# Kernel optimization log

Measured on AMD Instinct MI355X. Metric: run time of the kernel, lower is better.

The kernel has to match this reference:

```python
import jax, jax.numpy as jnp
import numpy as np


def _conv2d(x, w, b):
    # NCHW valid conv, kernel shape OIHW
    y = jax.lax.conv_general_dilated(x, w, (1, 1), 'VALID',
                                     dimension_numbers=('NCHW', 'OIHW', 'NCHW'))
    return y + b[None, :, None, None]


def _rgcn(x, src, dst, edge_type, root, rel, bias):
    # PyG RGCNConv: out_i = x_i @ root + bias + sum_r mean_{j in N_r(i)} x_j @ W_r
    # x: [B, N, F]; src/dst: [E]; rel: [R, F, F]
    out = x @ root + bias
    N = x.shape[1]
    for r in range(rel.shape[0]):  # small fixed relation count
        m = (edge_type == r).astype(x.dtype)                # [E]
        msg = (x @ rel[r])[:, src] * m[None, :, None]       # [B, E, F]
        agg = jnp.zeros_like(out).at[:, dst].add(msg)       # [B, N, F]
        cnt = jnp.zeros((N,), x.dtype).at[dst].add(m)       # per-node relation degree
        out = out + agg / jnp.clip(cnt, 1.0)[None, :, None]
    return out


def setup_inputs() -> dict:
    key = jax.random.key(0)
    ks = jax.random.split(key, 16)
    B, C, N, T = 16, 3, 3000, 50
    E, R, S, F = 96000, 3, 500, 43  # F = 2*20 + 3
    observation = jax.random.normal(ks[0], (B, C, N, T), jnp.float32)
    last_action = jax.random.uniform(ks[1], (B, S + 1), dtype=jnp.float32)
    edge_index = jax.random.randint(ks[2], (2, E), 0, N, jnp.int32)
    edge_type = jax.random.randint(ks[3], (E,), 0, R, jnp.int32)
    nodes_to_select = jnp.sort(jax.random.randint(ks[4], (S,), 0, N, jnp.int32))

    def w(k, shape, fan_in):
        return jax.random.normal(k, shape, jnp.float32) / np.sqrt(fan_in).astype(np.float32)

    params = dict(
        ws1=w(ks[5], (3, 3, 1, 3), 9), bs1=jnp.zeros(3, jnp.float32),
        ws2=w(ks[6], (20, 3, 1, 48), 144), bs2=jnp.zeros(20, jnp.float32),
        wm1=w(ks[7], (3, 3, 1, 21), 63), bm1=jnp.zeros(3, jnp.float32),
        wm2=w(ks[8], (20, 3, 1, 30), 90), bm2=jnp.zeros(20, jnp.float32),
        root1=w(ks[9], (F, F), F), rel1=w(ks[10], (R, F, F), F), bias1=jnp.zeros(F, jnp.float32),
        root2=w(ks[11], (F, F), F), rel2=w(ks[12], (R, F, F), F), bias2=jnp.zeros(F, jnp.float32),
        wf=w(ks[13], (1, 87, 1, 1), 87), bf=jnp.zeros(1, jnp.float32),
    )
    return {"observation": observation, "last_action": last_action,
            "edge_index": edge_index, "edge_type": edge_type,
            "nodes_to_select": nodes_to_select, **params}


def reference(observation, last_action, edge_index, edge_type, nodes_to_select,
              ws1, bs1, ws2, bs2, wm1, bm1, wm2, bm2,
              root1, rel1, bias1, root2, rel2, bias2, wf, bf):
    relu = jax.nn.relu
    B = observation.shape[0]
    last_stocks = last_action[:, 1:][:, None, :, None]                      # [B,1,S,1]
    short = relu(_conv2d(relu(_conv2d(observation, ws1, bs1)), ws2, bs2))   # [B,20,N,1]
    mid = relu(_conv2d(relu(_conv2d(observation, wm1, bm1)), wm2, bm2))     # [B,20,N,1]
    longf = relu(jnp.max(observation, axis=3, keepdims=True))               # [B,3,N,1]
    temporal = jnp.concatenate([short, mid, longf], axis=1)                 # [B,43,N,1]
    x = jnp.transpose(temporal[..., 0], (0, 2, 1))                          # [B,N,43]
    src, dst = edge_index[0], edge_index[1]
    h = jax.nn.leaky_relu(_rgcn(x, src, dst, edge_type, root1, rel1, bias1), 0.01)
    h = jax.nn.leaky_relu(_rgcn(h, src, dst, edge_type, root2, rel2, bias2), 0.01)
    graph_features = jnp.transpose(h, (0, 2, 1))[..., None]                 # [B,43,N,1]
    feats = jnp.concatenate([temporal, graph_features], axis=1)             # [B,86,N,1]
    feats = feats[:, :, nodes_to_select, :]                                 # [B,86,S,1]
    feats = jnp.concatenate([last_stocks, feats], axis=1)                   # [B,87,S,1]
    out = _conv2d(feats, wf, bf)                                            # [B,1,S,1]
    cash = jnp.zeros((B, 1, 1, 1), out.dtype)  # cash bias zeroed in mu()
    logits = jnp.concatenate([cash, out], axis=2)[:, 0, :, 0]               # [B,S+1]
    return jax.nn.softmax(logits, axis=-1)  # softmax_temperature = 1
```

## Files before the change

kernel.cpp:

```cpp
#include <hip/hip_runtime.h>
#include <math.h>

#define NB 16
#define NC 3
#define NN 3000
#define NT 50
#define NE 96000
#define NR 3
#define NS 500
#define NF 43
#define NFP 44
#define NBF (NB*NFP)
#define NBKT (NR*NN)
#define CAP 96

#define XT_OFF   0
#define H1_OFF   (XT_OFF + NN*NBF)
#define LG_OFF   (H1_OFF + NN*NBF)
#define INT_BASE (LG_OFF + NB*(NS+1))
#define CNT_OFF  0
#define EBUF_OFF (CNT_OFF + NBKT)

__global__ __launch_bounds__(256, 3) void k_front(
    const float* __restrict__ obs,
    const float* __restrict__ ws1, const float* __restrict__ bs1,
    const float* __restrict__ ws2, const float* __restrict__ bs2,
    const float* __restrict__ wm1, const float* __restrict__ bm1,
    const float* __restrict__ wm2, const float* __restrict__ bm2,
    float* __restrict__ x,
    const int* __restrict__ ei, const int* __restrict__ et,
    int* __restrict__ cnt, int* __restrict__ ebuf)
{
    __shared__ float sp[4][64][23];
    int tid = threadIdx.x;

    if (blockIdx.x >= 1500) {
        int e = (blockIdx.x - 1500) * 256 + tid;
        int bkt = et[e] * NN + ei[NE + e];
        int pos = atomicAdd(&cnt[bkt], 1);
        if (pos < CAP) ebuf[bkt * CAP + pos] = ei[e];
        return;
    }

    int wave = __builtin_amdgcn_readfirstlane(tid >> 6);
    int lane = tid & 63;

    if (blockIdx.x < 750) {
        int idx = blockIdx.x * 64 + lane;
        int b = idx / NN, n = idx - b * NN;
        float wS[3][14];
        int base = 12 * wave;
        #pragma unroll
        for (int c = 0; c < 3; ++c) {
            const float2* p2 = (const float2*)(obs + ((size_t)(b * NC + c) * NN + n) * NT + base);
            #pragma unroll
            for (int jj = 0; jj < 7; ++jj) {
                float2 u = p2[jj];
                wS[c][2 * jj] = u.x; wS[c][2 * jj + 1] = u.y;
            }
        }
        float acc[20];
        #pragma unroll
        for (int o = 0; o < 20; ++o) acc[o] = 0.f;
        #pragma unroll
        for (int j = 0; j < 12; ++j) {
            float y[3];
            #pragma unroll
            for (int c = 0; c < 3; ++c) {
                float s = bs1[c];
                #pragma unroll
                for (int i = 0; i < 3; ++i)
                    #pragma unroll
                    for (int k = 0; k < 3; ++k)
                        s = fmaf(wS[i][j + k], ws1[(c * 3 + i) * 3 + k], s);
                y[c] = fmaxf(s, 0.f);
            }
            int gt = base + j;
            #pragma unroll
            for (int o = 0; o < 20; ++o) {
                float a = acc[o];
                #pragma unroll
                for (int c = 0; c < 3; ++c)
                    a = fmaf(y[c], ws2[(o * 3 + c) * 48 + gt], a);
                acc[o] = a;
            }
        }
        #pragma unroll
        for (int o = 0; o < 20; ++o) sp[wave][lane][o] = acc[o];
        __syncthreads();
        #pragma unroll
        for (int q = 0; q < 5; ++q) {
            int item = q * 256 + tid;
            int node = item / 20, o = item - node * 20;
            int g = blockIdx.x * 64 + node;
            int bb = g / NN, nn = g - bb * NN;
            float s = ((sp[0][node][o] + sp[1][node][o]) +
                       (sp[2][node][o] + sp[3][node][o])) + bs2[o];
            x[(size_t)nn * NBF + bb * NFP + o] = fmaxf(s, 0.f);
        }
        return;
    }

    {
        int idx = (blockIdx.x - 750) * 64 + lane;
        int b = idx / NN, n = idx - b * NN;
        int mbase = (wave < 3) ? 8 * wave : 24;
        int nld   = (wave < 3) ? 14 : 13;
        const float* orow = obs + ((size_t)b * NC * NN + n) * NT + mbase;

        float s[3][8];
        #pragma unroll
        for (int c = 0; c < 3; ++c)
            #pragma unroll
            for (int t = 0; t < 8; ++t) s[c][t] = bm1[c];
        float cmax[3];
        float wA[28], wB[28];

        #define LOADW(buf, ch)                                                  \
        {                                                                       \
            const float2* p2 = (const float2*)(orow + (size_t)(ch) * NN * NT);  \
            _Pragma("unroll")                                                   \
            for (int jj = 0; jj < 14; ++jj) {                                   \
                if (jj < nld) {                                                 \
                    float2 u = p2[jj];                                          \
                    buf[2 * jj] = u.x; buf[2 * jj + 1] = u.y;                   \
                } else { buf[2 * jj] = 0.f; buf[2 * jj + 1] = 0.f; }            \
            }                                                                   \
        }
        #define COMPW(buf, ii)                                                  \
        {                                                                       \
            float m = buf[0];                                                   \
            _Pragma("unroll")                                                   \
            for (int t = 1; t < 28; ++t) m = fmaxf(m, buf[t]);                  \
            cmax[ii] = m;                                                       \
            _Pragma("unroll")                                                   \
            for (int c = 0; c < 3; ++c)                                         \
                _Pragma("unroll")                                               \
                for (int t = 0; t < 8; ++t) {                                   \
                    float a = s[c][t];                                          \
                    _Pragma("unroll")                                           \
                    for (int k = 0; k < 21; ++k)                                \
                        a = fmaf(buf[t + k], wm1[(c * 3 + (ii)) * 21 + k], a);  \
                    s[c][t] = a;                                                \
                }                                                               \
        }

        LOADW(wA, 0)
        LOADW(wB, 1)
        COMPW(wA, 0)
        LOADW(wA, 2)
        COMPW(wB, 1)
        COMPW(wA, 2)
        #undef LOADW
        #undef COMPW

        float acc[20];
        #pragma unroll
        for (int o = 0; o < 20; ++o) acc[o] = 0.f;
        int cntM = (wave < 3) ? 8 : 6;
        #pragma unroll
        for (int j = 0; j < 8; ++j) {
            if (j < cntM) {
                float y0 = fmaxf(s[0][j], 0.f);
                float y1 = fmaxf(s[1][j], 0.f);
                float y2 = fmaxf(s[2][j], 0.f);
                int gt = mbase + j;
                #pragma unroll
                for (int o = 0; o < 20; ++o) {
                    float a = acc[o];
                    a = fmaf(y0, wm2[(o * 3 + 0) * 30 + gt], a);
                    a = fmaf(y1, wm2[(o * 3 + 1) * 30 + gt], a);
                    a = fmaf(y2, wm2[(o * 3 + 2) * 30 + gt], a);
                    acc[o] = a;
                }
            }
        }
        #pragma unroll
        for (int o = 0; o < 20; ++o) sp[wave][lane][o] = acc[o];
        #pragma unroll
        for (int c = 0; c < 3; ++c) sp[wave][lane][20 + c] = cmax[c];
    }
    __syncthreads();
    #pragma unroll
    for (int q = 0; q < 6; ++q) {
        int item = q * 256 + tid;
        if (item < 1472) {
            int node = item / 23, o = item - node * 23;
            int g = (blockIdx.x - 750) * 64 + node;
            int bb = g / NN, nn = g - bb * NN;
            size_t row = (size_t)nn * NBF + bb * NFP;
            if (o < 20) {
                float s = ((sp[0][node][o] + sp[1][node][o]) +
                           (sp[2][node][o] + sp[3][node][o])) + bm2[o];
                x[row + 20 + o] = fmaxf(s, 0.f);
            } else {
                float m = fmaxf(fmaxf(sp[0][node][o], sp[1][node][o]),
                                fmaxf(sp[2][node][o], sp[3][node][o]));
                x[row + 40 + (o - 20)] = fmaxf(m, 0.f);
            }
        }
    }
}

template<bool LEAKY, bool SEL>
__global__ __launch_bounds__(256) void k_rgcn(
    const float* __restrict__ in, const float* __restrict__ xsrc,
    const int* __restrict__ cnt, const int* __restrict__ ebuf,
    const int* __restrict__ sel,
    const float* __restrict__ root, const float* __restrict__ rel,
    const float* __restrict__ bias,
    const float* __restrict__ la, const float* __restrict__ wf,
    const float* __restrict__ bf,
    float* __restrict__ out)
{
    __shared__ float lrow[4][NBF];
    __shared__ float sP[8][4][NFP];

    int tid = threadIdx.x;
    int wave = __builtin_amdgcn_readfirstlane(tid >> 6);
    int lane = tid & 63;
    int i = blockIdx.x;
    int node = __builtin_amdgcn_readfirstlane(SEL ? sel[i] : i);

    const float* wbase = (wave == 0) ? root : (rel + (size_t)(wave - 1) * NF * NF);
    float wsl[43];
    #pragma unroll
    for (int j = 0; j < 43; ++j)
        wsl[j] = (lane < NF) ? wbase[j * NF + lane] : 0.f;

    if (wave == 3) {
        #pragma unroll
        for (int j = 0; j < 11; ++j) {
            float v = in[(size_t)node * NBF + j * 64 + lane];
            if (LEAKY) v = v >= 0.f ? v : 0.01f * v;
            lrow[0][j * 64 + lane] = v;
        }
    } else {
        int bkt = wave * NN + node;
        int cvr = __builtin_amdgcn_readfirstlane(cnt[bkt]);
        float ic = 1.0f / fmaxf((float)cvr, 1.0f);
        int cv = cvr > CAP ? CAP : cvr;
        const int* eb = ebuf + bkt * CAP;

        float acc[11];
        #pragma unroll
        for (int j = 0; j < 11; ++j) acc[j] = 0.f;

        for (int e = 0; e < cv; e += 4) {
            int4 q = *(const int4*)(eb + e);
            int m = cv - e;
            {
                const float* p = in + (size_t)__builtin_amdgcn_readfirstlane(q.x) * NBF;
                #pragma unroll
                for (int j = 0; j < 11; ++j) {
                    float v = p[j * 64 + lane];
                    if (LEAKY) v = v >= 0.f ? v : 0.01f * v;
                    acc[j] += v;
                }
            }
            if (m > 1) {
                const float* p = in + (size_t)__builtin_amdgcn_readfirstlane(q.y) * NBF;
                #pragma unroll
                for (int j = 0; j < 11; ++j) {
                    float v = p[j * 64 + lane];
                    if (LEAKY) v = v >= 0.f ? v : 0.01f * v;
                    acc[j] += v;
                }
            }
            if (m > 2) {
                const float* p = in + (size_t)__builtin_amdgcn_readfirstlane(q.z) * NBF;
                #pragma unroll
                for (int j = 0; j < 11; ++j) {
                    float v = p[j * 64 + lane];
                    if (LEAKY) v = v >= 0.f ? v : 0.01f * v;
                    acc[j] += v;
                }
            }
            if (m > 3) {
                const float* p = in + (size_t)__builtin_amdgcn_readfirstlane(q.w) * NBF;
                #pragma unroll
                for (int j = 0; j < 11; ++j) {
                    float v = p[j * 64 + lane];
                    if (LEAKY) v = v >= 0.f ? v : 0.01f * v;
                    acc[j] += v;
                }
            }
        }
        #pragma unroll
        for (int j = 0; j < 11; ++j) lrow[wave + 1][j * 64 + lane] = acc[j] * ic;
    }
    __syncthreads();

    for (int h = 0; h < 2; ++h) {
        #pragma unroll
        for (int rr = 0; rr < 8; ++rr) {
            int b = h * 8 + rr;
            const float4* a4 = (const float4*)&lrow[wave][b * NFP];
            float a0 = 0.f, a1 = 0.f, a2 = 0.f, a3 = 0.f;
            #pragma unroll
            for (int c = 0; c < 10; ++c) {
                float4 v = a4[c];
                a0 = fmaf(v.x, wsl[4 * c], a0);
                a1 = fmaf(v.y, wsl[4 * c + 1], a1);
                a2 = fmaf(v.z, wsl[4 * c + 2], a2);
                a3 = fmaf(v.w, wsl[4 * c + 3], a3);
            }
            {
                float4 v = a4[10];
                a0 = fmaf(v.x, wsl[40], a0);
                a1 = fmaf(v.y, wsl[41], a1);
                a2 = fmaf(v.z, wsl[42], a2);
            }
            if (lane < NF) sP[rr][wave][lane] = (a0 + a1) + (a2 + a3);
        }
        __syncthreads();

        int r0 = 2 * wave, r1 = 2 * wave + 1;
        int b0 = h * 8 + r0, b1 = h * 8 + r1;
        if (!SEL) {
            if (lane < NF) {
                float bi_ = bias[lane];
                float s0 = ((sP[r0][0][lane] + sP[r0][1][lane]) +
                            (sP[r0][2][lane] + sP[r0][3][lane])) + bi_;
                float s1 = ((sP[r1][0][lane] + sP[r1][1][lane]) +
                            (sP[r1][2][lane] + sP[r1][3][lane])) + bi_;
                out[(size_t)i * NBF + b0 * NFP + lane] = s0;
                out[(size_t)i * NBF + b1 * NFP + lane] = s1;
            }
        } else {
            float p0 = 0.f, p1 = 0.f;
            if (lane < NF) {
                float bi_ = bias[lane];
                float s0 = ((sP[r0][0][lane] + sP[r0][1][lane]) +
                            (sP[r0][2][lane] + sP[r0][3][lane])) + bi_;
                float s1 = ((sP[r1][0][lane] + sP[r1][1][lane]) +
                            (sP[r1][2][lane] + sP[r1][3][lane])) + bi_;
                s0 = s0 >= 0.f ? s0 : 0.01f * s0;
                s1 = s1 >= 0.f ? s1 : 0.01f * s1;
                float x0 = xsrc[(size_t)node * NBF + b0 * NFP + lane];
                float x1 = xsrc[(size_t)node * NBF + b1 * NFP + lane];
                p0 = fmaf(wf[44 + lane], s0, wf[1 + lane] * x0);
                p1 = fmaf(wf[44 + lane], s1, wf[1 + lane] * x1);
            }
            #pragma unroll
            for (int o = 32; o > 0; o >>= 1) {
                p0 += __shfl_down(p0, o);
                p1 += __shfl_down(p1, o);
            }
            if (lane == 0) {
                out[(size_t)b0 * (NS + 1) + 1 + i] =
                    p0 + bf[0] + wf[0] * la[b0 * (NS + 1) + 1 + i];
                out[(size_t)b1 * (NS + 1) + 1 + i] =
                    p1 + bf[0] + wf[0] * la[b1 * (NS + 1) + 1 + i];
            }
        }
        __syncthreads();
    }
}

__device__ inline float wred_max(float v) {
    #pragma unroll
    for (int o = 32; o > 0; o >>= 1) v = fmaxf(v, __shfl_down(v, o));
    return v;
}
__device__ inline float wred_sum(float v) {
    #pragma unroll
    for (int o = 32; o > 0; o >>= 1) v += __shfl_down(v, o);
    return v;
}

__global__ __launch_bounds__(512) void k_softmax(
    const float* __restrict__ lg, float* __restrict__ out)
{
    __shared__ float sred[8];
    __shared__ float sbc[2];
    int b = blockIdx.x, tid = threadIdx.x;

    float val = -3.0e38f;
    if (tid <= NS) val = (tid == 0) ? 0.f : lg[(size_t)b * (NS + 1) + tid];

    float m = wred_max(val);
    if ((tid & 63) == 0) sred[tid >> 6] = m;
    __syncthreads();
    if (tid == 0) {
        float mm = sred[0];
        #pragma unroll
        for (int i = 1; i < 8; ++i) mm = fmaxf(mm, sred[i]);
        sbc[0] = mm;
    }
    __syncthreads();
    float mx = sbc[0];
    float e = (tid <= NS) ? expf(val - mx) : 0.f;
    float s = wred_sum(e);
    if ((tid & 63) == 0) sred[tid >> 6] = s;
    __syncthreads();
    if (tid == 0) {
        float t = 0.f;
        #pragma unroll
        for (int i = 0; i < 8; ++i) t += sred[i];
        sbc[1] = t;
    }
    __syncthreads();
    if (tid <= NS) out[(size_t)b * (NS + 1) + tid] = e / sbc[1];
}

extern "C" void kernel_launch(void* const* d_in, const int* in_sizes, int n_in,
                              void* d_out, int out_size, void* d_ws, size_t ws_size,
                              hipStream_t stream)
{
    const float* obs   = (const float*)d_in[0];
    const float* la    = (const float*)d_in[1];
    const int*   ei    = (const int*)d_in[2];
    const int*   et    = (const int*)d_in[3];
    const int*   nodes = (const int*)d_in[4];
    const float* ws1 = (const float*)d_in[5],  *bs1 = (const float*)d_in[6];
    const float* ws2 = (const float*)d_in[7],  *bs2 = (const float*)d_in[8];
    const float* wm1 = (const float*)d_in[9],  *bm1 = (const float*)d_in[10];
    const float* wm2 = (const float*)d_in[11], *bm2 = (const float*)d_in[12];
    const float* root1 = (const float*)d_in[13], *rel1 = (const float*)d_in[14], *bias1 = (const float*)d_in[15];
    const float* root2 = (const float*)d_in[16], *rel2 = (const float*)d_in[17], *bias2 = (const float*)d_in[18];
    const float* wf = (const float*)d_in[19], *bf = (const float*)d_in[20];

    float* wsp = (float*)d_ws;
    float* x   = wsp + XT_OFF;
    float* h1  = wsp + H1_OFF;
    float* lg  = wsp + LG_OFF;
    int*   ibase = (int*)(wsp + INT_BASE);
    int*   cnt   = ibase + CNT_OFF;
    int*   ebuf  = ibase + EBUF_OFF;

    hipMemsetAsync(cnt, 0, NBKT * sizeof(int), stream);

    k_front<<<1875, 256, 0, stream>>>(
        obs, ws1, bs1, ws2, bs2, wm1, bm1, wm2, bm2, x, ei, et, cnt, ebuf);

    k_rgcn<false, false><<<NN, 256, 0, stream>>>(
        x, nullptr, cnt, ebuf, nullptr, root1, rel1, bias1,
        nullptr, nullptr, nullptr, h1);

    k_rgcn<true, true><<<NS, 256, 0, stream>>>(
        h1, x, cnt, ebuf, nodes, root2, rel2, bias2,
        la, wf, bf, lg);

    k_softmax<<<NB, 512, 0, stream>>>(lg, (float*)d_out);
}
```

Before: 210.3 us.

## Split neighbor aggregation across all waves and fuse softmax into last RGCN block

Previously one wave per relation gathered whole neighbor rows while the fourth wave only loaded the self row. Now all four waves share every relation's gather, each lane covering up to three columns of the 704-wide row and looping over the relations, which balances load across waves. The separate softmax kernel is removed. The last block of the selected-node RGCN, detected by an atomic counter plus threadfence, computes the softmax directly. This saves a launch at the cost of a serialized tail block and an extra counter in the memset.

```diff
diff --git a/kernel.cpp b/kernel.cpp
--- a/kernel.cpp
+++ b/kernel.cpp
@@ -19,7 +19,8 @@
 #define LG_OFF   (H1_OFF + NN*NBF)
 #define INT_BASE (LG_OFF + NB*(NS+1))
 #define CNT_OFF  0
-#define EBUF_OFF (CNT_OFF + NBKT)
+#define DONE_OFF NBKT
+#define EBUF_OFF (NBKT + 4)
 
 __global__ __launch_bounds__(256, 3) void k_front(
     const float* __restrict__ obs,
@@ -211,10 +212,12 @@
     const float* __restrict__ bias,
     const float* __restrict__ la, const float* __restrict__ wf,
     const float* __restrict__ bf,
-    float* __restrict__ out)
+    float* __restrict__ out, int* __restrict__ done,
+    float* __restrict__ res)
 {
     __shared__ float lrow[4][NBF];
     __shared__ float sP[8][4][NFP];
+    __shared__ int slast;
 
     int tid = threadIdx.x;
     int wave = __builtin_amdgcn_readfirstlane(tid >> 6);
@@ -228,67 +231,60 @@
     for (int j = 0; j < 43; ++j)
         wsl[j] = (lane < NF) ? wbase[j * NF + lane] : 0.f;
 
-    if (wave == 3) {
-        #pragma unroll
-        for (int j = 0; j < 11; ++j) {
-            float v = in[(size_t)node * NBF + j * 64 + lane];
-            if (LEAKY) v = v >= 0.f ? v : 0.01f * v;
-            lrow[0][j * 64 + lane] = v;
-        }
-    } else {
-        int bkt = wave * NN + node;
+    int base = wave * 64 + lane;
+    bool has3 = (wave < 3);
+
+    #define ACT(v) (LEAKY ? ((v) >= 0.f ? (v) : 0.01f * (v)) : (v))
+    {
+        const float* p = in + (size_t)node * NBF;
+        float v0 = p[base], v1 = p[base + 256];
+        float v2 = has3 ? p[base + 512] : 0.f;
+        lrow[0][base] = ACT(v0);
+        lrow[0][base + 256] = ACT(v1);
+        if (has3) lrow[0][base + 512] = ACT(v2);
+    }
+    #pragma unroll 1
+    for (int r = 0; r < NR; ++r) {
+        int bkt = r * NN + node;
         int cvr = __builtin_amdgcn_readfirstlane(cnt[bkt]);
         float ic = 1.0f / fmaxf((float)cvr, 1.0f);
         int cv = cvr > CAP ? CAP : cvr;
         const int* eb = ebuf + bkt * CAP;
 
-        float acc[11];
-        #pragma unroll
-        for (int j = 0; j < 11; ++j) acc[j] = 0.f;
-
+        float a0 = 0.f, a1 = 0.f, a2 = 0.f;
         for (int e = 0; e < cv; e += 4) {
             int4 q = *(const int4*)(eb + e);
             int m = cv - e;
             {
                 const float* p = in + (size_t)__builtin_amdgcn_readfirstlane(q.x) * NBF;
-                #pragma unroll
-                for (int j = 0; j < 11; ++j) {
-                    float v = p[j * 64 + lane];
-                    if (LEAKY) v = v >= 0.f ? v : 0.01f * v;
-                    acc[j] += v;
-                }
+                float u0 = p[base], u1 = p[base + 256];
+                a0 += ACT(u0); a1 += ACT(u1);
+                if (has3) { float u2 = p[base + 512]; a2 += ACT(u2); }
             }
             if (m > 1) {
                 const float* p = in + (size_t)__builtin_amdgcn_readfirstlane(q.y) * NBF;
-                #pragma unroll
-                for (int j = 0; j < 11; ++j) {
-                    float v = p[j * 64 + lane];
-                    if (LEAKY) v = v >= 0.f ? v : 0.01f * v;
-                    acc[j] += v;
-                }
+                float u0 = p[base], u1 = p[base + 256];
+                a0 += ACT(u0); a1 += ACT(u1);
+                if (has3) { float u2 = p[base + 512]; a2 += ACT(u2); }
             }
             if (m > 2) {
                 const float* p = in + (size_t)__builtin_amdgcn_readfirstlane(q.z) * NBF;
-                #pragma unroll
-                for (int j = 0; j < 11; ++j) {
-                    float v = p[j * 64 + lane];
-                    if (LEAKY) v = v >= 0.f ? v : 0.01f * v;
-                    acc[j] += v;
-                }
+                float u0 = p[base], u1 = p[base + 256];
+                a0 += ACT(u0); a1 += ACT(u1);
+                if (has3) { float u2 = p[base + 512]; a2 += ACT(u2); }
             }
             if (m > 3) {
                 const float* p = in + (size_t)__builtin_amdgcn_readfirstlane(q.w) * NBF;
-                #pragma unroll
-                for (int j = 0; j < 11; ++j) {
-                    float v = p[j * 64 + lane];
-                    if (LEAKY) v = v >= 0.f ? v : 0.01f * v;
-                    acc[j] += v;
-                }
-            }
-        }
-        #pragma unroll
-        for (int j = 0; j < 11; ++j) lrow[wave + 1][j * 64 + lane] = acc[j] * ic;
-    }
+                float u0 = p[base], u1 = p[base + 256];
+                a0 += ACT(u0); a1 += ACT(u1);
+                if (has3) { float u2 = p[base + 512]; a2 += ACT(u2); }
+            }
+        }
+        lrow[r + 1][base] = a0 * ic;
+        lrow[r + 1][base + 256] = a1 * ic;
+        if (has3) lrow[r + 1][base + 512] = a2 * ic;
+    }
+    #undef ACT
     __syncthreads();
 
     for (int h = 0; h < 2; ++h) {
@@ -356,52 +352,46 @@
         }
         __syncthreads();
     }
-}
-
-__device__ inline float wred_max(float v) {
-    #pragma unroll
-    for (int o = 32; o > 0; o >>= 1) v = fmaxf(v, __shfl_down(v, o));
-    return v;
-}
-__device__ inline float wred_sum(float v) {
-    #pragma unroll
-    for (int o = 32; o > 0; o >>= 1) v += __shfl_down(v, o);
-    return v;
-}
-
-__global__ __launch_bounds__(512) void k_softmax(
-    const float* __restrict__ lg, float* __restrict__ out)
-{
-    __shared__ float sred[8];
-    __shared__ float sbc[2];
-    int b = blockIdx.x, tid = threadIdx.x;
-
-    float val = -3.0e38f;
-    if (tid <= NS) val = (tid == 0) ? 0.f : lg[(size_t)b * (NS + 1) + tid];
-
-    float m = wred_max(val);
-    if ((tid & 63) == 0) sred[tid >> 6] = m;
-    __syncthreads();
-    if (tid == 0) {
-        float mm = sred[0];
-        #pragma unroll
-        for (int i = 1; i < 8; ++i) mm = fmaxf(mm, sred[i]);
-        sbc[0] = mm;
-    }
-    __syncthreads();
-    float mx = sbc[0];
-    float e = (tid <= NS) ? expf(val - mx) : 0.f;
-    float s = wred_sum(e);
-    if ((tid & 63) == 0) sred[tid >> 6] = s;
-    __syncthreads();
-    if (tid == 0) {
-        float t = 0.f;
-        #pragma unroll
-        for (int i = 0; i < 8; ++i) t += sred[i];
-        sbc[1] = t;
-    }
-    __syncthreads();
-    if (tid <= NS) out[(size_t)b * (NS + 1) + tid] = e / sbc[1];
+
+    if (SEL) {
+        __threadfence();
+        if (tid == 0) {
+            int old = atomicAdd(done, 1);
+            slast = (old == NS - 1) ? 1 : 0;
+        }
+        __syncthreads();
+        if (slast) {
+            __threadfence();
+            for (int bb = wave; bb < NB; bb += 4) {
+                const float* l = out + (size_t)bb * (NS + 1);
+                float vals[8]; float mx = -3.0e38f;
+                #pragma unroll
+                for (int k = 0; k < 8; ++k) {
+                    int idx = k * 64 + lane;
+                    float v = (idx == 0) ? 0.f
+                            : ((idx <= NS) ? l[idx] : -3.0e38f);
+                    vals[k] = v; mx = fmaxf(mx, v);
+                }
+                #pragma unroll
+                for (int o = 32; o > 0; o >>= 1) mx = fmaxf(mx, __shfl_xor(mx, o));
+                float ev[8]; float se = 0.f;
+                #pragma unroll
+                for (int k = 0; k < 8; ++k) {
+                    int idx = k * 64 + lane;
+                    float e = (idx <= NS) ? expf(vals[k] - mx) : 0.f;
+                    ev[k] = e; se += e;
+                }
+                #pragma unroll
+                for (int o = 32; o > 0; o >>= 1) se += __shfl_xor(se, o);
+                float inv = 1.f / se;
+                #pragma unroll
+                for (int k = 0; k < 8; ++k) {
+                    int idx = k * 64 + lane;
+                    if (idx <= NS) res[(size_t)bb * (NS + 1) + idx] = ev[k] * inv;
+                }
+            }
+        }
+    }
 }
 
 extern "C" void kernel_launch(void* const* d_in, const int* in_sizes, int n_in,
@@ -427,20 +417,19 @@
     float* lg  = wsp + LG_OFF;
     int*   ibase = (int*)(wsp + INT_BASE);
     int*   cnt   = ibase + CNT_OFF;
+    int*   done  = ibase + DONE_OFF;
     int*   ebuf  = ibase + EBUF_OFF;
 
-    hipMemsetAsync(cnt, 0, NBKT * sizeof(int), stream);
+    hipMemsetAsync(cnt, 0, (NBKT + 4) * sizeof(int), stream);
 
     k_front<<<1875, 256, 0, stream>>>(
         obs, ws1, bs1, ws2, bs2, wm1, bm1, wm2, bm2, x, ei, et, cnt, ebuf);
 
     k_rgcn<false, false><<<NN, 256, 0, stream>>>(
         x, nullptr, cnt, ebuf, nullptr, root1, rel1, bias1,
-        nullptr, nullptr, nullptr, h1);
+        nullptr, nullptr, nullptr, h1, done, nullptr);
 
     k_rgcn<true, true><<<NS, 256, 0, stream>>>(
         h1, x, cnt, ebuf, nodes, root2, rel2, bias2,
-        la, wf, bf, lg);
-
-    k_softmax<<<NB, 512, 0, stream>>>(lg, (float*)d_out);
+        la, wf, bf, lg, done, (float*)d_out);
 }
```

Measured after the change: 275.7 us. +31.1%, slower.

## Double waves per RGCN block, splitting edge gathers across wave pairs

Applied to the files above, without the earlier changes.

The RGCN kernel moves from 4 to 8 waves per block. Each relation's neighbour gather is split across two waves that take alternating groups of four edges, and the self-row load gets its own wave. In the transform phase each wave handles 8 of the 16 batches, so the old two-pass batch loop and its extra barriers go away. This cuts the serial gather latency per block, which is the critical path when nodes have many edges. In exchange it uses more LDS and registers per block (43 weight registers per thread), which may reduce occupancy, and wave 7 sits idle during the gather.

```diff
diff --git a/kernel.cpp b/kernel.cpp
--- a/kernel.cpp
+++ b/kernel.cpp
@@ -203,7 +203,7 @@
 }
 
 template<bool LEAKY, bool SEL>
-__global__ __launch_bounds__(256) void k_rgcn(
+__global__ __launch_bounds__(512) void k_rgcn(
     const float* __restrict__ in, const float* __restrict__ xsrc,
     const int* __restrict__ cnt, const int* __restrict__ ebuf,
     const int* __restrict__ sel,
@@ -213,8 +213,9 @@
     const float* __restrict__ bf,
     float* __restrict__ out)
 {
-    __shared__ float lrow[4][NBF];
-    __shared__ float sP[8][4][NFP];
+    __shared__ float lself[NBF];
+    __shared__ float lz[6][NBF];
+    __shared__ float sP[16][4][NFP];
 
     int tid = threadIdx.x;
     int wave = __builtin_amdgcn_readfirstlane(tid >> 6);
@@ -222,21 +223,23 @@
     int i = blockIdx.x;
     int node = __builtin_amdgcn_readfirstlane(SEL ? sel[i] : i);
 
-    const float* wbase = (wave == 0) ? root : (rel + (size_t)(wave - 1) * NF * NF);
+    int m = wave & 3;
+    const float* wbase = (m == 0) ? root : (rel + (size_t)(m - 1) * NF * NF);
     float wsl[43];
     #pragma unroll
     for (int j = 0; j < 43; ++j)
         wsl[j] = (lane < NF) ? wbase[j * NF + lane] : 0.f;
 
-    if (wave == 3) {
+    #define ACT(v) (LEAKY ? ((v) >= 0.f ? (v) : 0.01f * (v)) : (v))
+    if (wave == 6) {
         #pragma unroll
         for (int j = 0; j < 11; ++j) {
             float v = in[(size_t)node * NBF + j * 64 + lane];
-            if (LEAKY) v = v >= 0.f ? v : 0.01f * v;
-            lrow[0][j * 64 + lane] = v;
-        }
-    } else {
-        int bkt = wave * NN + node;
+            lself[j * 64 + lane] = ACT(v);
+        }
+    } else if (wave < 6) {
+        int r = wave >> 1, h = wave & 1;
+        int bkt = r * NN + node;
         int cvr = __builtin_amdgcn_readfirstlane(cnt[bkt]);
         float ic = 1.0f / fmaxf((float)cvr, 1.0f);
         int cv = cvr > CAP ? CAP : cvr;
@@ -246,57 +249,43 @@
         #pragma unroll
         for (int j = 0; j < 11; ++j) acc[j] = 0.f;
 
-        for (int e = 0; e < cv; e += 4) {
+        for (int e = h * 4; e < cv; e += 8) {
             int4 q = *(const int4*)(eb + e);
-            int m = cv - e;
+            int mm = cv - e;
             {
                 const float* p = in + (size_t)__builtin_amdgcn_readfirstlane(q.x) * NBF;
                 #pragma unroll
-                for (int j = 0; j < 11; ++j) {
-                    float v = p[j * 64 + lane];
-                    if (LEAKY) v = v >= 0.f ? v : 0.01f * v;
-                    acc[j] += v;
-                }
-            }
-            if (m > 1) {
+                for (int j = 0; j < 11; ++j) { float v = p[j * 64 + lane]; acc[j] += ACT(v); }
+            }
+            if (mm > 1) {
                 const float* p = in + (size_t)__builtin_amdgcn_readfirstlane(q.y) * NBF;
                 #pragma unroll
-                for (int j = 0; j < 11; ++j) {
-                    float v = p[j * 64 + lane];
-                    if (LEAKY) v = v >= 0.f ? v : 0.01f * v;
-                    acc[j] += v;
-                }
-            }
-            if (m > 2) {
+                for (int j = 0; j < 11; ++j) { float v = p[j * 64 + lane]; acc[j] += ACT(v); }
+            }
+            if (mm > 2) {
                 const float* p = in + (size_t)__builtin_amdgcn_readfirstlane(q.z) * NBF;
                 #pragma unroll
-                for (int j = 0; j < 11; ++j) {
-                    float v = p[j * 64 + lane];
-                    if (LEAKY) v = v >= 0.f ? v : 0.01f * v;
-                    acc[j] += v;
-                }
-            }
-            if (m > 3) {
+                for (int j = 0; j < 11; ++j) { float v = p[j * 64 + lane]; acc[j] += ACT(v); }
+            }
+            if (mm > 3) {
                 const float* p = in + (size_t)__builtin_amdgcn_readfirstlane(q.w) * NBF;
                 #pragma unroll
-                for (int j = 0; j < 11; ++j) {
-                    float v = p[j * 64 + lane];
-                    if (LEAKY) v = v >= 0.f ? v : 0.01f * v;
-                    acc[j] += v;
-                }
-            }
-        }
-        #pragma unroll
-        for (int j = 0; j < 11; ++j) lrow[wave + 1][j * 64 + lane] = acc[j] * ic;
-    }
-    __syncthreads();
-
-    for (int h = 0; h < 2; ++h) {
-        #pragma unroll
-        for (int rr = 0; rr < 8; ++rr) {
-            int b = h * 8 + rr;
-            const float4* a4 = (const float4*)&lrow[wave][b * NFP];
-            float a0 = 0.f, a1 = 0.f, a2 = 0.f, a3 = 0.f;
+                for (int j = 0; j < 11; ++j) { float v = p[j * 64 + lane]; acc[j] += ACT(v); }
+            }
+        }
+        #pragma unroll
+        for (int j = 0; j < 11; ++j) lz[wave][j * 64 + lane] = acc[j] * ic;
+    }
+    #undef ACT
+    __syncthreads();
+
+    int hb = wave >> 2;
+    #pragma unroll
+    for (int rr = 0; rr < 8; ++rr) {
+        int b = hb * 8 + rr;
+        float a0 = 0.f, a1 = 0.f, a2 = 0.f, a3 = 0.f;
+        if (m == 0) {
+            const float4* a4 = (const float4*)&lself[b * NFP];
             #pragma unroll
             for (int c = 0; c < 10; ++c) {
                 float4 v = a4[c];
@@ -305,56 +294,67 @@
                 a2 = fmaf(v.z, wsl[4 * c + 2], a2);
                 a3 = fmaf(v.w, wsl[4 * c + 3], a3);
             }
-            {
-                float4 v = a4[10];
-                a0 = fmaf(v.x, wsl[40], a0);
-                a1 = fmaf(v.y, wsl[41], a1);
-                a2 = fmaf(v.z, wsl[42], a2);
-            }
-            if (lane < NF) sP[rr][wave][lane] = (a0 + a1) + (a2 + a3);
-        }
-        __syncthreads();
-
-        int r0 = 2 * wave, r1 = 2 * wave + 1;
-        int b0 = h * 8 + r0, b1 = h * 8 + r1;
-        if (!SEL) {
-            if (lane < NF) {
-                float bi_ = bias[lane];
-                float s0 = ((sP[r0][0][lane] + sP[r0][1][lane]) +
-                            (sP[r0][2][lane] + sP[r0][3][lane])) + bi_;
-                float s1 = ((sP[r1][0][lane] + sP[r1][1][lane]) +
-                            (sP[r1][2][lane] + sP[r1][3][lane])) + bi_;
-                out[(size_t)i * NBF + b0 * NFP + lane] = s0;
-                out[(size_t)i * NBF + b1 * NFP + lane] = s1;
-            }
+            float4 v = a4[10];
+            a0 = fmaf(v.x, wsl[40], a0);
+            a1 = fmaf(v.y, wsl[41], a1);
+            a2 = fmaf(v.z, wsl[42], a2);
         } else {
-            float p0 = 0.f, p1 = 0.f;
-            if (lane < NF) {
-                float bi_ = bias[lane];
-                float s0 = ((sP[r0][0][lane] + sP[r0][1][lane]) +
-                            (sP[r0][2][lane] + sP[r0][3][lane])) + bi_;
-                float s1 = ((sP[r1][0][lane] + sP[r1][1][lane]) +
-                            (sP[r1][2][lane] + sP[r1][3][lane])) + bi_;
-                s0 = s0 >= 0.f ? s0 : 0.01f * s0;
-                s1 = s1 >= 0.f ? s1 : 0.01f * s1;
-                float x0 = xsrc[(size_t)node * NBF + b0 * NFP + lane];
-                float x1 = xsrc[(size_t)node * NBF + b1 * NFP + lane];
-                p0 = fmaf(wf[44 + lane], s0, wf[1 + lane] * x0);
-                p1 = fmaf(wf[44 + lane], s1, wf[1 + lane] * x1);
-            }
-            #pragma unroll
-            for (int o = 32; o > 0; o >>= 1) {
-                p0 += __shfl_down(p0, o);
-                p1 += __shfl_down(p1, o);
-            }
-            if (lane == 0) {
-                out[(size_t)b0 * (NS + 1) + 1 + i] =
-                    p0 + bf[0] + wf[0] * la[b0 * (NS + 1) + 1 + i];
-                out[(size_t)b1 * (NS + 1) + 1 + i] =
-                    p1 + bf[0] + wf[0] * la[b1 * (NS + 1) + 1 + i];
-            }
-        }
-        __syncthreads();
+            const float4* pa = (const float4*)&lz[2 * (m - 1)][b * NFP];
+            const float4* pb = (const float4*)&lz[2 * (m - 1) + 1][b * NFP];
+            #pragma unroll
+            for (int c = 0; c < 10; ++c) {
+                float4 u = pa[c], t = pb[c];
+                a0 = fmaf(u.x + t.x, wsl[4 * c], a0);
+                a1 = fmaf(u.y + t.y, wsl[4 * c + 1], a1);
+                a2 = fmaf(u.z + t.z, wsl[4 * c + 2], a2);
+                a3 = fmaf(u.w + t.w, wsl[4 * c + 3], a3);
+            }
+            float4 u = pa[10], t = pb[10];
+            a0 = fmaf(u.x + t.x, wsl[40], a0);
+            a1 = fmaf(u.y + t.y, wsl[41], a1);
+            a2 = fmaf(u.z + t.z, wsl[42], a2);
+        }
+        if (lane < NF) sP[b][m][lane] = (a0 + a1) + (a2 + a3);
+    }
+    __syncthreads();
+
+    int b0 = 2 * wave, b1 = 2 * wave + 1;
+    if (!SEL) {
+        if (lane < NF) {
+            float bi_ = bias[lane];
+            float s0 = ((sP[b0][0][lane] + sP[b0][1][lane]) +
+                        (sP[b0][2][lane] + sP[b0][3][lane])) + bi_;
+            float s1 = ((sP[b1][0][lane] + sP[b1][1][lane]) +
+                        (sP[b1][2][lane] + sP[b1][3][lane])) + bi_;
+            out[(size_t)i * NBF + b0 * NFP + lane] = s0;
+            out[(size_t)i * NBF + b1 * NFP + lane] = s1;
+        }
+    } else {
+        float p0 = 0.f, p1 = 0.f;
+        if (lane < NF) {
+            float bi_ = bias[lane];
+            float s0 = ((sP[b0][0][lane] + sP[b0][1][lane]) +
+                        (sP[b0][2][lane] + sP[b0][3][lane])) + bi_;
+            float s1 = ((sP[b1][0][lane] + sP[b1][1][lane]) +
+                        (sP[b1][2][lane] + sP[b1][3][lane])) + bi_;
+            s0 = s0 >= 0.f ? s0 : 0.01f * s0;
+            s1 = s1 >= 0.f ? s1 : 0.01f * s1;
+            float x0 = xsrc[(size_t)node * NBF + b0 * NFP + lane];
+            float x1 = xsrc[(size_t)node * NBF + b1 * NFP + lane];
+            p0 = fmaf(wf[44 + lane], s0, wf[1 + lane] * x0);
+            p1 = fmaf(wf[44 + lane], s1, wf[1 + lane] * x1);
+        }
+        #pragma unroll
+        for (int o = 32; o > 0; o >>= 1) {
+            p0 += __shfl_down(p0, o);
+            p1 += __shfl_down(p1, o);
+        }
+        if (lane == 0) {
+            out[(size_t)b0 * (NS + 1) + 1 + i] =
+                p0 + bf[0] + wf[0] * la[b0 * (NS + 1) + 1 + i];
+            out[(size_t)b1 * (NS + 1) + 1 + i] =
+                p1 + bf[0] + wf[0] * la[b1 * (NS + 1) + 1 + i];
+        }
     }
 }
 
@@ -434,11 +434,11 @@
     k_front<<<1875, 256, 0, stream>>>(
         obs, ws1, bs1, ws2, bs2, wm1, bm1, wm2, bm2, x, ei, et, cnt, ebuf);
 
-    k_rgcn<false, false><<<NN, 256, 0, stream>>>(
+    k_rgcn<false, false><<<NN, 512, 0, stream>>>(
         x, nullptr, cnt, ebuf, nullptr, root1, rel1, bias1,
         nullptr, nullptr, nullptr, h1);
 
-    k_rgcn<true, true><<<NS, 256, 0, stream>>>(
+    k_rgcn<true, true><<<NS, 512, 0, stream>>>(
         h1, x, cnt, ebuf, nodes, root2, rel2, bias2,
         la, wf, bf, lg);
 
```

New measurement: 236.5 us. 12.5% more time.
